# Optimization experiments

Measured on AMD Instinct MI355X. Metric: run time of the kernel, lower is better.

Reference implementation:

```python
import jax, jax.numpy as jnp
import numpy as np

N, S, A, D = 2048, 4096, 4, 2


def setup_inputs() -> dict:
    key = jax.random.key(0)
    k1, k2 = jax.random.split(key, 2)
    # one-hot DNA sequences: tokens in [0, A)
    tokens_NxS = jax.random.randint(k1, (N, S), 0, A)
    data_NxSxA = jax.nn.one_hot(tokens_NxS, A, dtype=jnp.float32)
    # learnable per-sequence embedding table (EmbeddingTableSequenceEncoder)
    table_ND = jax.random.normal(k2, (N, D), dtype=jnp.float32) * 0.1
    # Hyperbolic distance learnable log-scale, initial scale 0.1
    log_scale = jnp.asarray(np.log(0.1), dtype=jnp.float32)
    return {"data_NxSxA": data_NxSxA, "table_ND": table_ND, "log_scale": log_scale}


def _hamming_NxN(data_NxSxA):
    # rows are one-hot, so per-site equality over A <=> dot product == 1
    s = jnp.float32(data_NxSxA.shape[1])
    matches_NxN = jnp.einsum("isa,jsa->ij", data_NxSxA, data_NxSxA)
    return (s - matches_NxN) / s


def _normalize(v_NxD):
    # softly clamp into the open unit ball via tanh on the norm
    norms_Nx1 = jnp.linalg.norm(v_NxD, axis=-1, keepdims=True)
    return v_NxD / jnp.maximum(norms_Nx1, 1e-12) * jnp.tanh(norms_Nx1)


def _hyperbolic_dist_NxN(table_ND, log_scale):
    z_ND = _normalize(table_ND)
    sq_norm_N = jnp.sum(z_ND * z_ND, axis=-1)            # ||z_i||^2
    diff_sq_NxN = jnp.sum((z_ND[:, None, :] - z_ND[None, :, :]) ** 2, axis=-1)
    denom_NxN = (1.0 - sq_norm_N)[:, None] * (1.0 - sq_norm_N)[None, :]
    arg_NxN = 1.0 + 2.0 * diff_sq_NxN / denom_NxN
    # clamp for numerical safety at the diagonal (arg == 1 exactly)
    dist_NxN = jnp.arccosh(jnp.maximum(arg_NxN, 1.0 + 1e-7))
    return dist_NxN * jnp.exp(log_scale)


def reference(data_NxSxA, table_ND, log_scale):
    hamming_NxN = _hamming_NxN(data_NxSxA)
    embed_NxN = _hyperbolic_dist_NxN(table_ND, log_scale)
    return jnp.mean((hamming_NxN - embed_NxN) ** 2)
```

## Files before the change

kernel.cpp:

```cpp
#include <hip/hip_runtime.h>

#define N_SEQ 2048
#define S_LEN 4096
#define W_SEQ 64
#define TILE 64
#define T_TILES (N_SEQ / TILE)
#define NBLK (T_TILES * (T_TILES + 1) / 2)
#define CHUNK 16
#define STRIDE 17

__global__ __launch_bounds__(256) void encode_kernel(const float4* __restrict__ data,
                                                     ulonglong2* __restrict__ codes) {
    int t = blockIdx.x * 256 + threadIdx.x;
    float4 v = data[t];
    int c = (int)(v.y + 2.0f * v.z + 3.0f * v.w + 0.5f);
    unsigned long long lo = __ballot(c & 1);
    unsigned long long hi = __ballot(c & 2);
    if ((threadIdx.x & 63) == 0) {
        ulonglong2 e; e.x = lo; e.y = hi;
        codes[t >> 6] = e;
    }
}

__global__ void zprep_kernel(const float* __restrict__ table, float4* __restrict__ zbuf) {
    int i = blockIdx.x * blockDim.x + threadIdx.x;
    if (i >= N_SEQ) return;
    float vx = table[2 * i], vy = table[2 * i + 1];
    float n = sqrtf(vx * vx + vy * vy);
    float f = tanhf(n) / fmaxf(n, 1e-12f);
    float zx = vx * f, zy = vy * f;
    float omn = 1.0f - (zx * zx + zy * zy);
    zbuf[i] = make_float4(zx, zy, omn, 0.0f);
}

__global__ __launch_bounds__(256) void pairs_kernel(const ulonglong2* __restrict__ codes,
                                                    const float4* __restrict__ zbuf,
                                                    const float* __restrict__ log_scale,
                                                    double* __restrict__ partials) {
    __shared__ ulonglong2 As[TILE * STRIDE];
    __shared__ ulonglong2 Bs[TILE * STRIDE];
    __shared__ float wsum[4];

    int b = blockIdx.x;
    int r = (int)((sqrtf(8.0f * (float)b + 1.0f) - 1.0f) * 0.5f);
    while ((r + 1) * (r + 2) / 2 <= b) ++r;
    while (r * (r + 1) / 2 > b) --r;
    int c = b - r * (r + 1) / 2;
    int i0 = c * TILE, j0 = r * TILE;

    int tid = threadIdx.x;
    int tx = tid & 15, ty = tid >> 4;

    int mis[4][4];
#pragma unroll
    for (int k = 0; k < 4; ++k)
#pragma unroll
        for (int l = 0; l < 4; ++l) mis[k][l] = 0;

    for (int cc = 0; cc < W_SEQ / CHUNK; ++cc) {
#pragma unroll
        for (int p = 0; p < 4; ++p) {
            int e = tid + p * 256;
            int row = e >> 4, w = e & 15;
            As[row * STRIDE + w] = codes[(i0 + row) * W_SEQ + cc * CHUNK + w];
            Bs[row * STRIDE + w] = codes[(j0 + row) * W_SEQ + cc * CHUNK + w];
        }
        __syncthreads();
#pragma unroll
        for (int w = 0; w < CHUNK; ++w) {
            ulonglong2 a[4], bb[4];
#pragma unroll
            for (int k = 0; k < 4; ++k) a[k] = As[(ty + 16 * k) * STRIDE + w];
#pragma unroll
            for (int l = 0; l < 4; ++l) bb[l] = Bs[(tx + 16 * l) * STRIDE + w];
#pragma unroll
            for (int k = 0; k < 4; ++k)
#pragma unroll
                for (int l = 0; l < 4; ++l)
                    mis[k][l] += __popcll((a[k].x ^ bb[l].x) | (a[k].y ^ bb[l].y));
        }
        __syncthreads();
    }

    float scale = expf(log_scale[0]);
    const float inv_s = 1.0f / (float)S_LEN;
    float local = 0.0f;
#pragma unroll
    for (int k = 0; k < 4; ++k) {
        int i = i0 + ty + 16 * k;
        float4 zi = zbuf[i];
#pragma unroll
        for (int l = 0; l < 4; ++l) {
            int j = j0 + tx + 16 * l;
            float4 zj = zbuf[j];
            float ham = (float)mis[k][l] * inv_s;
            float dx = zi.x - zj.x, dy = zi.y - zj.y;
            float dsq = dx * dx + dy * dy;
            float arg = 1.0f + 2.0f * dsq / (zi.z * zj.z);
            arg = fmaxf(arg, 1.0f + 1e-7f);
            float dist = acoshf(arg) * scale;
            float d = ham - dist;
            float wgt = (i < j) ? 2.0f : (i == j ? 1.0f : 0.0f);
            local += wgt * d * d;
        }
    }

#pragma unroll
    for (int off = 32; off > 0; off >>= 1) local += __shfl_down(local, off);
    if ((tid & 63) == 0) wsum[tid >> 6] = local;
    __syncthreads();
    if (tid == 0)
        partials[blockIdx.x] = (double)(wsum[0] + wsum[1] + wsum[2] + wsum[3]);
}

__global__ void finalize_kernel(const double* __restrict__ partials, float* __restrict__ out) {
    __shared__ double ws[4];
    int tid = threadIdx.x;
    double s = 0.0;
    for (int k = tid; k < NBLK; k += 256) s += partials[k];
#pragma unroll
    for (int off = 32; off > 0; off >>= 1) s += __shfl_down(s, off);
    if ((tid & 63) == 0) ws[tid >> 6] = s;
    __syncthreads();
    if (tid == 0) {
        double tot = ws[0] + ws[1] + ws[2] + ws[3];
        out[0] = (float)(tot / ((double)N_SEQ * (double)N_SEQ));
    }
}

extern "C" void kernel_launch(void* const* d_in, const int* in_sizes, int n_in,
                              void* d_out, int out_size, void* d_ws, size_t ws_size,
                              hipStream_t stream) {
    const float4* data      = (const float4*)d_in[0];
    const float*  table     = (const float*)d_in[1];
    const float*  log_scale = (const float*)d_in[2];
    float* out = (float*)d_out;

    char* ws = (char*)d_ws;
    ulonglong2* codes    = (ulonglong2*)ws;
    float4*     zbuf     = (float4*)(ws + (size_t)N_SEQ * W_SEQ * sizeof(ulonglong2));
    double*     partials = (double*)((char*)zbuf + (size_t)N_SEQ * sizeof(float4));

    encode_kernel  <<<N_SEQ * S_LEN / 256, 256, 0, stream>>>(data, codes);
    zprep_kernel   <<<(N_SEQ + 255) / 256, 256, 0, stream>>>(table, zbuf);
    pairs_kernel   <<<NBLK, 256, 0, stream>>>(codes, zbuf, log_scale, partials);
    finalize_kernel<<<1, 256, 0, stream>>>(partials, out);
}
```

Baseline: 250.9 us.

## Fuse zprep into encode, grid-stride encode, and finalize via atomic last-block

```diff
diff --git a/kernel.cpp b/kernel.cpp
--- a/kernel.cpp
+++ b/kernel.cpp
@@ -8,44 +8,57 @@
 #define NBLK (T_TILES * (T_TILES + 1) / 2)
 #define CHUNK 16
 #define STRIDE 17
+#define NSITES (N_SEQ * S_LEN)
+#define ENC_BLOCKS 4096
+#define ENC_THREADS (ENC_BLOCKS * 256)
 
 __global__ __launch_bounds__(256) void encode_kernel(const float4* __restrict__ data,
-                                                     ulonglong2* __restrict__ codes) {
-    int t = blockIdx.x * 256 + threadIdx.x;
-    float4 v = data[t];
-    int c = (int)(v.y + 2.0f * v.z + 3.0f * v.w + 0.5f);
-    unsigned long long lo = __ballot(c & 1);
-    unsigned long long hi = __ballot(c & 2);
-    if ((threadIdx.x & 63) == 0) {
-        ulonglong2 e; e.x = lo; e.y = hi;
-        codes[t >> 6] = e;
+                                                     const float* __restrict__ table,
+                                                     ulonglong2* __restrict__ codes,
+                                                     float4* __restrict__ zbuf,
+                                                     double* __restrict__ acc,
+                                                     unsigned* __restrict__ counter) {
+    int tid = threadIdx.x;
+    int gtid = blockIdx.x * 256 + tid;
+
+    if (gtid == 0) { *acc = 0.0; *counter = 0u; }
+
+    if (gtid < N_SEQ) {
+        float vx = table[2 * gtid], vy = table[2 * gtid + 1];
+        float n = sqrtf(vx * vx + vy * vy);
+        float f = tanhf(n) / fmaxf(n, 1e-12f);
+        float zx = vx * f, zy = vy * f;
+        float omn = 1.0f - (zx * zx + zy * zy);
+        zbuf[gtid] = make_float4(zx, zy, omn, 0.0f);
     }
-}
 
-__global__ void zprep_kernel(const float* __restrict__ table, float4* __restrict__ zbuf) {
-    int i = blockIdx.x * blockDim.x + threadIdx.x;
-    if (i >= N_SEQ) return;
-    float vx = table[2 * i], vy = table[2 * i + 1];
-    float n = sqrtf(vx * vx + vy * vy);
-    float f = tanhf(n) / fmaxf(n, 1e-12f);
-    float zx = vx * f, zy = vy * f;
-    float omn = 1.0f - (zx * zx + zy * zy);
-    zbuf[i] = make_float4(zx, zy, omn, 0.0f);
+    for (int t = gtid; t < NSITES; t += ENC_THREADS) {
+        float4 v = data[t];
+        int c = (int)(v.y + 2.0f * v.z + 3.0f * v.w + 0.5f);
+        unsigned long long lo = __ballot(c & 1);
+        unsigned long long hi = __ballot(c & 2);
+        if ((tid & 63) == 0) {
+            ulonglong2 e; e.x = lo; e.y = hi;
+            codes[t >> 6] = e;
+        }
+    }
 }
 
 __global__ __launch_bounds__(256) void pairs_kernel(const ulonglong2* __restrict__ codes,
                                                     const float4* __restrict__ zbuf,
                                                     const float* __restrict__ log_scale,
-                                                    double* __restrict__ partials) {
+                                                    double* __restrict__ acc,
+                                                    unsigned* __restrict__ counter,
+                                                    float* __restrict__ out) {
     __shared__ ulonglong2 As[TILE * STRIDE];
     __shared__ ulonglong2 Bs[TILE * STRIDE];
     __shared__ float wsum[4];
 
-    int b = blockIdx.x;
-    int r = (int)((sqrtf(8.0f * (float)b + 1.0f) - 1.0f) * 0.5f);
-    while ((r + 1) * (r + 2) / 2 <= b) ++r;
-    while (r * (r + 1) / 2 > b) --r;
-    int c = b - r * (r + 1) / 2;
+    int bid = blockIdx.x;
+    int r = (int)((sqrtf(8.0f * (float)bid + 1.0f) - 1.0f) * 0.5f);
+    while ((r + 1) * (r + 2) / 2 <= bid) ++r;
+    while (r * (r + 1) / 2 > bid) --r;
+    int c = bid - r * (r + 1) / 2;
     int i0 = c * TILE, j0 = r * TILE;
 
     int tid = threadIdx.x;
@@ -109,22 +122,16 @@
     for (int off = 32; off > 0; off >>= 1) local += __shfl_down(local, off);
     if ((tid & 63) == 0) wsum[tid >> 6] = local;
     __syncthreads();
-    if (tid == 0)
-        partials[blockIdx.x] = (double)(wsum[0] + wsum[1] + wsum[2] + wsum[3]);
-}
 
-__global__ void finalize_kernel(const double* __restrict__ partials, float* __restrict__ out) {
-    __shared__ double ws[4];
-    int tid = threadIdx.x;
-    double s = 0.0;
-    for (int k = tid; k < NBLK; k += 256) s += partials[k];
-#pragma unroll
-    for (int off = 32; off > 0; off >>= 1) s += __shfl_down(s, off);
-    if ((tid & 63) == 0) ws[tid >> 6] = s;
-    __syncthreads();
     if (tid == 0) {
-        double tot = ws[0] + ws[1] + ws[2] + ws[3];
-        out[0] = (float)(tot / ((double)N_SEQ * (double)N_SEQ));
+        double part = (double)(wsum[0] + wsum[1] + wsum[2] + wsum[3]);
+        atomicAdd(acc, part);
+        __threadfence();
+        unsigned prev = atomicAdd(counter, 1u);
+        if (prev == NBLK - 1) {
+            double tot = atomicAdd(acc, 0.0);
+            out[0] = (float)(tot / ((double)N_SEQ * (double)N_SEQ));
+        }
     }
 }
 
@@ -137,12 +144,11 @@
     float* out = (float*)d_out;
 
     char* ws = (char*)d_ws;
-    ulonglong2* codes    = (ulonglong2*)ws;
-    float4*     zbuf     = (float4*)(ws + (size_t)N_SEQ * W_SEQ * sizeof(ulonglong2));
-    double*     partials = (double*)((char*)zbuf + (size_t)N_SEQ * sizeof(float4));
+    ulonglong2* codes   = (ulonglong2*)ws;
+    float4*     zbuf    = (float4*)(ws + (size_t)N_SEQ * W_SEQ * sizeof(ulonglong2));
+    double*     acc     = (double*)((char*)zbuf + (size_t)N_SEQ * sizeof(float4));
+    unsigned*   counter = (unsigned*)((char*)acc + sizeof(double));
 
-    encode_kernel  <<<N_SEQ * S_LEN / 256, 256, 0, stream>>>(data, codes);
-    zprep_kernel   <<<(N_SEQ + 255) / 256, 256, 0, stream>>>(table, zbuf);
-    pairs_kernel   <<<NBLK, 256, 0, stream>>>(codes, zbuf, log_scale, partials);
-    finalize_kernel<<<1, 256, 0, stream>>>(partials, out);
+    encode_kernel<<<ENC_BLOCKS, 256, 0, stream>>>(data, table, codes, zbuf, acc, counter);
+    pairs_kernel <<<NBLK,       256, 0, stream>>>(codes, zbuf, log_scale, acc, counter, out);
 }
```

Measured after the change: 253.8 us. About the same (+1.1%).
